# Performance work log

Measured on AMD Instinct MI355X. Metric: run time of the kernel, lower is better.

The kernel has to match this reference:

```python
import jax, jax.numpy as jnp
import numpy as np

DIM = 1024
HEADS = 32
HEAD_DIM = DIM // HEADS
SR_RATIO = 2
N_RATIO = SR_RATIO * SR_RATIO  # AvgPool1d kernel/stride
BN_EPS = 1e-6


def setup_inputs() -> dict:
    key = jax.random.key(0)
    ks = jax.random.split(key, 10)
    B, N, C = 4, 2048, DIM
    s = C ** -0.5
    return {
        "x": jax.random.normal(ks[0], (B, N, C), dtype=jnp.float32),
        # torch.nn.Linear weights, shape [out, in]; applied as x @ W.T
        "Wq": jax.random.normal(ks[1], (C, C), dtype=jnp.float32) * s,
        "Wk": jax.random.normal(ks[2], (C, C), dtype=jnp.float32) * s,
        "Wv": jax.random.normal(ks[3], (C, C), dtype=jnp.float32) * s,
        "Wp": jax.random.normal(ks[4], (C, C), dtype=jnp.float32) * s,
        "bp": jax.random.normal(ks[5], (C,), dtype=jnp.float32) * 0.01,
        # BatchNorm1d (eval mode) affine + running stats over channel dim C
        "bn_gamma": jnp.ones((C,), dtype=jnp.float32),
        "bn_beta": jnp.zeros((C,), dtype=jnp.float32),
        "bn_mean": jax.random.normal(ks[6], (C,), dtype=jnp.float32) * 0.01,
        "bn_var": jnp.ones((C,), dtype=jnp.float32) + jax.random.uniform(ks[7], (C,), dtype=jnp.float32) * 0.1,
    }


def reference(x, Wq, Wk, Wv, Wp, bp, bn_gamma, bn_beta, bn_mean, bn_var):
    B, N, C = x.shape
    scale = HEAD_DIM ** -0.5
    # Q from full-resolution tokens
    q = (x @ Wq.T).reshape(B, N, HEADS, HEAD_DIM).transpose(0, 2, 1, 3)  # [B,H,N,d]
    # spatial reduction: AvgPool1d(kernel=N_RATIO, stride=N_RATIO) over tokens
    xr = x.reshape(B, N // N_RATIO, N_RATIO, C).mean(axis=2)  # [B,M,C]
    # BatchNorm1d eval: normalize channel dim with running stats
    xr = (xr - bn_mean) * jax.lax.rsqrt(bn_var + BN_EPS) * bn_gamma + bn_beta
    M = xr.shape[1]
    k = (xr @ Wk.T).reshape(B, M, HEADS, HEAD_DIM).transpose(0, 2, 1, 3)  # [B,H,M,d]
    v = (xr @ Wv.T).reshape(B, M, HEADS, HEAD_DIM).transpose(0, 2, 1, 3)  # [B,H,M,d]
    # NOTE: no softmax in the original module — raw scaled scores feed the second matmul
    attn = jnp.einsum("bhnd,bhmd->bhnm", q, k) * scale  # [B,H,N,M]
    out = jnp.einsum("bhnm,bhmd->bhnd", attn, v)        # [B,H,N,d]
    out = out.transpose(0, 2, 1, 3).reshape(B, N, C)
    return out @ Wp.T + bp
```

## Files before the change

### kernel.cpp

```cpp
#include <hip/hip_runtime.h>
#include <stdint.h>

#define DEVFN __device__ __forceinline__

typedef __attribute__((ext_vector_type(8))) short s16x8;
typedef __attribute__((ext_vector_type(4))) float f32x4;

DEVFN float bf2f(uint16_t u) {
  union { uint32_t i; float f; } v; v.i = ((uint32_t)u) << 16; return v.f;
}
DEVFN uint16_t f2bf(float f) {
  union { float f; uint32_t i; } v; v.f = f;
  uint32_t u = v.i;
  return (uint16_t)((u + 0x7FFFu + ((u >> 16) & 1u)) >> 16);
}

DEVFN void gload_lds16(const void* g, void* l) {
  __builtin_amdgcn_global_load_lds(
      (const __attribute__((address_space(1))) uint32_t*)g,
      (__attribute__((address_space(3))) uint32_t*)l, 16, 0, 0);
}

__global__ __launch_bounds__(256)
void prep_kernel(const float* __restrict__ x,
                 const float* __restrict__ bn_g, const float* __restrict__ bn_b,
                 const float* __restrict__ bn_m, const float* __restrict__ bn_v,
                 const float* __restrict__ Wk, const float* __restrict__ Wv,
                 const float* __restrict__ Wp,
                 uint16_t* __restrict__ Xh,
                 uint16_t* __restrict__ XRh,
                 uint16_t* __restrict__ Wkvi,
                 uint16_t* __restrict__ Wph)
{
  const int t = threadIdx.x;
  const int bid = blockIdx.x;
  if (bid < 2048) {
    const int prow = bid;
    const int c0 = t * 4;
    const size_t xbase = (size_t)prow * 4096 + c0;
    float s[4] = {0.f, 0.f, 0.f, 0.f};
#pragma unroll
    for (int r = 0; r < 4; ++r) {
      const float4 w = *(const float4*)(x + xbase + (size_t)r * 1024);
      const float vv[4] = { w.x, w.y, w.z, w.w };
      uint64_t wh = 0;
#pragma unroll
      for (int j = 0; j < 4; ++j) {
        wh |= ((uint64_t)f2bf(vv[j])) << (16 * j);
        s[j] += vv[j];
      }
      *(uint64_t*)(Xh + xbase + (size_t)r * 1024) = wh;
    }
    uint64_t wh = 0;
#pragma unroll
    for (int j = 0; j < 4; ++j) {
      const int c = c0 + j;
      const float y = (s[j] * 0.25f - bn_m[c]) / sqrtf(bn_v[c] + 1e-6f) * bn_g[c] + bn_b[c];
      wh |= ((uint64_t)f2bf(y)) << (16 * j);
    }
    *(uint64_t*)(XRh + (size_t)prow * 1024 + c0) = wh;
  } else {
    const int wb = bid - 2048;
    const int which = wb >> 10;
    const int i = (wb & 1023) * 256 + t;
    const float* src = (which == 0) ? Wk : (which == 1) ? Wv : Wp;
    const float4 v = ((const float4*)src)[i];
    const float vv[4] = { v.x, v.y, v.z, v.w };
    uint64_t wh = 0;
#pragma unroll
    for (int j = 0; j < 4; ++j)
      wh |= ((uint64_t)f2bf(vv[j])) << (16 * j);
    if (which == 2) {
      ((uint64_t*)Wph)[i] = wh;
    } else {
      const int row  = i >> 8;
      const int col4 = i & 255;
      const int nrow = ((row >> 5) << 6) + which * 32 + (row & 31);
      ((uint64_t*)Wkvi)[(size_t)nrow * 256 + col4] = wh;
    }
  }
}

template<int APARTS, int BPARTS, bool BATCHB, bool AMODA, int EPI, bool KSPLIT2,
         bool SMALLM>
__global__ __launch_bounds__(256, 2)
void gemm_nt(const uint16_t* __restrict__ A0, const uint16_t* __restrict__ A1,
             const uint16_t* __restrict__ B0, const uint16_t* __restrict__ B1,
             float* __restrict__ C32, uint16_t* __restrict__ Cb0,
             const float* __restrict__ bias,
             int M, int N, int K, int rows_per_batch)
{
  constexpr int BM = SMALLM ? 64 : 128, BN = 128, BK = 64;
  constexpr int WCN = SMALLM ? 4 : 2;
  constexpr int WNW = BN / WCN;
  constexpr int NREP = WNW / 16;
  constexpr int APASS = SMALLM ? 2 : 4;
  __shared__ uint16_t sA[APARTS][BM * BK];
  __shared__ uint16_t sB[BPARTS][BN * BK];

  const int t = threadIdx.x;
  const int lane = t & 63;
  const int wave = t >> 6;
  const int wr = wave / WCN, wc = wave % WCN;
  const int fq = lane >> 4, fr = lane & 15;

  const int nwg = gridDim.x;
  const int cpx = nwg >> 3;
  const int orig = blockIdx.x;
  const int swz = (orig & 7) * cpx + (orig >> 3);
  const int nbx = N >> 7;
  const int bm = (swz / nbx) * BM;
  const int bn = (swz % nbx) * BN;

  const uint16_t* Ap[2] = { A0, A1 };
  const uint16_t* Bp[2] = { B0, B1 };
  if (BATCHB) {
    const size_t boff = (size_t)(bm / rows_per_batch) * (size_t)N * (size_t)K;
    Bp[0] += boff;
    if (BPARTS > 1) Bp[1] += boff;
  }
  if (KSPLIT2) {
    const size_t half = (size_t)blockIdx.y * M * N;
    if (EPI == 1) Cb0 += half; else C32 += half;
  }

  f32x4 acc[4][NREP];
#pragma unroll
  for (int m = 0; m < 4; ++m)
#pragma unroll
    for (int n = 0; n < NREP; ++n) acc[m][n] = (f32x4)0.0f;

  const int nkt = K >> (KSPLIT2 ? 7 : 6);
  const int kt0 = KSPLIT2 ? (blockIdx.y * nkt) : 0;
  for (int kt = kt0; kt < kt0 + nkt; ++kt) {
    __syncthreads();
#pragma unroll
    for (int i = 0; i < APASS; ++i) {
      const int X = t * 16 + i * 4096;
      const int r = X >> 7;
      const int g = ((X >> 4) & 7) ^ (r & 7);
      const int kcol = (kt << 6) + g * 8;
      const int arow = AMODA ? ((bm + r) & 1023) : (bm + r);
      const size_t srcA = (size_t)arow * K + kcol;
#pragma unroll
      for (int p = 0; p < APARTS; ++p)
        gload_lds16(Ap[p] + srcA, (char*)(&sA[p][0]) + X);
    }
#pragma unroll
    for (int i = 0; i < 4; ++i) {
      const int X = t * 16 + i * 4096;
      const int r = X >> 7;
      const int g = ((X >> 4) & 7) ^ (r & 7);
      const int kcol = (kt << 6) + g * 8;
      const size_t srcB = (size_t)(bn + r) * K + kcol;
#pragma unroll
      for (int p = 0; p < BPARTS; ++p)
        gload_lds16(Bp[p] + srcB, (char*)(&sB[p][0]) + X);
    }
    __syncthreads();
#pragma unroll
    for (int ks = 0; ks < 2; ++ks) {
      s16x8 av[APARTS][4], bv[BPARTS][NREP];
#pragma unroll
      for (int m = 0; m < 4; ++m) {
        const int ra = wr * 64 + m * 16 + fr;
        const int offA = ra * 128 + ((((ks << 2) + fq) ^ (ra & 7)) << 4);
#pragma unroll
        for (int p = 0; p < APARTS; ++p)
          av[p][m] = *(const s16x8*)((const char*)(&sA[p][0]) + offA);
      }
#pragma unroll
      for (int n = 0; n < NREP; ++n) {
        const int rb = wc * WNW + n * 16 + fr;
        const int offB = rb * 128 + ((((ks << 2) + fq) ^ (rb & 7)) << 4);
#pragma unroll
        for (int p = 0; p < BPARTS; ++p)
          bv[p][n] = *(const s16x8*)((const char*)(&sB[p][0]) + offB);
      }
#pragma unroll
      for (int m = 0; m < 4; ++m)
#pragma unroll
        for (int n = 0; n < NREP; ++n) {
          acc[m][n] = __builtin_amdgcn_mfma_f32_16x16x32_bf16(
              av[0][m], bv[0][n], acc[m][n], 0, 0, 0);
          if constexpr (BPARTS > 1)
            acc[m][n] = __builtin_amdgcn_mfma_f32_16x16x32_bf16(
                av[0][m], bv[1][n], acc[m][n], 0, 0, 0);
          if constexpr (APARTS > 1)
            acc[m][n] = __builtin_amdgcn_mfma_f32_16x16x32_bf16(
                av[1][m], bv[0][n], acc[m][n], 0, 0, 0);
        }
    }
  }

#pragma unroll
  for (int m = 0; m < 4; ++m) {
#pragma unroll
    for (int n = 0; n < NREP; ++n) {
#pragma unroll
      for (int j = 0; j < 4; ++j) {
        const int row = bm + wr * 64 + m * 16 + fq * 4 + j;
        const int col = bn + wc * WNW + n * 16 + fr;
        const size_t idx = (size_t)row * N + col;
        float v = acc[m][n][j];
        if constexpr (EPI == 0) {
          C32[idx] = v;
        } else if constexpr (EPI == 1) {
          Cb0[idx] = f2bf(v);
        } else {
          C32[idx] = v + bias[col];
        }
      }
    }
  }
}

__global__ __launch_bounds__(256, 2)
void gemm_kv(const uint16_t* __restrict__ A,
             const uint16_t* __restrict__ B,
             float* __restrict__ part)
{
  constexpr int BM = 64, BN = 128, BK = 64;
  __shared__ union {
    struct { uint16_t a[BM * BK]; uint16_t b[BN * BK]; } s;
    float c[BM][BN];
  } sm;

  const int t = threadIdx.x;
  const int lane = t & 63;
  const int wave = t >> 6;
  const int wc = wave;
  const int fq = lane >> 4, fr = lane & 15;

  const int nwg = gridDim.x;
  const int cpx = nwg >> 3;
  const int orig = blockIdx.x;
  const int swz = (orig & 7) * cpx + (orig >> 3);
  const int bmI = swz >> 4;
  const int bnI = swz & 15;
  const int bm = bmI * BM;
  const int bn = bnI * BN;

  f32x4 acc[4][2];
#pragma unroll
  for (int m = 0; m < 4; ++m)
#pragma unroll
    for (int n = 0; n < 2; ++n) acc[m][n] = (f32x4)0.0f;

  for (int kt = 0; kt < 16; ++kt) {
    __syncthreads();
#pragma unroll
    for (int i = 0; i < 2; ++i) {
      const int X = t * 16 + i * 4096;
      const int r = X >> 7;
      const int g = ((X >> 4) & 7) ^ (r & 7);
      const int kcol = (kt << 6) + g * 8;
      gload_lds16(A + (size_t)(bm + r) * 1024 + kcol, (char*)(&sm.s.a[0]) + X);
    }
#pragma unroll
    for (int i = 0; i < 4; ++i) {
      const int X = t * 16 + i * 4096;
      const int r = X >> 7;
      const int g = ((X >> 4) & 7) ^ (r & 7);
      const int kcol = (kt << 6) + g * 8;
      gload_lds16(B + (size_t)(bn + r) * 1024 + kcol, (char*)(&sm.s.b[0]) + X);
    }
    __syncthreads();
#pragma unroll
    for (int ks = 0; ks < 2; ++ks) {
      s16x8 av[4], bv[2];
#pragma unroll
      for (int m = 0; m < 4; ++m) {
        const int ra = m * 16 + fr;
        const int offA = ra * 128 + ((((ks << 2) + fq) ^ (ra & 7)) << 4);
        av[m] = *(const s16x8*)((const char*)(&sm.s.a[0]) + offA);
      }
#pragma unroll
      for (int n = 0; n < 2; ++n) {
        const int rb = wc * 32 + n * 16 + fr;
        const int offB = rb * 128 + ((((ks << 2) + fq) ^ (rb & 7)) << 4);
        bv[n] = *(const s16x8*)((const char*)(&sm.s.b[0]) + offB);
      }
#pragma unroll
      for (int m = 0; m < 4; ++m)
#pragma unroll
        for (int n = 0; n < 2; ++n)
          acc[m][n] = __builtin_amdgcn_mfma_f32_16x16x32_bf16(
              av[m], bv[n], acc[m][n], 0, 0, 0);
    }
  }

  __syncthreads();
#pragma unroll
  for (int m = 0; m < 4; ++m)
#pragma unroll
    for (int n = 0; n < 2; ++n)
#pragma unroll
      for (int j = 0; j < 4; ++j) {
        const int row = m * 16 + fq * 4 + j;
        const int col = wc * 32 + n * 16 + fr;
        sm.c[row][col] = acc[m][n][j];
      }
  __syncthreads();

  const int hsel = t >> 7;
  const int f  = (t >> 2) & 31;
  const int e0 = (t & 3) * 8;
  const int kcol = hsel * 64 + f;
  const int vcol = hsel * 64 + 32 + e0;
  f32x4 a0 = (f32x4)0.0f, a1 = (f32x4)0.0f;
#pragma unroll 8
  for (int m = 0; m < 64; ++m) {
    const float kf = sm.c[m][kcol];
    const f32x4 v0 = *(const f32x4*)&sm.c[m][vcol];
    const f32x4 v1 = *(const f32x4*)&sm.c[m][vcol + 4];
    a0 += v0 * kf;
    a1 += v1 * kf;
  }
  const int b = bmI >> 3, ch = bmI & 7;
  const int h = bnI * 2 + hsel;
  float* o = part + (((size_t)(b * 32 + h) * 8 + ch) * 32 + f) * 32 + e0;
  *(f32x4*)o = a0;
  *(f32x4*)(o + 4) = a1;
}

__global__ __launch_bounds__(256)
void t_kernel(const float* __restrict__ part, const float* __restrict__ Wq,
              uint16_t* __restrict__ Tth)
{
  const int bid = blockIdx.x;
  const int b = bid >> 7, h = (bid >> 2) & 31, cc = bid & 3;
  const int bh = b * 32 + h;
  const int t = threadIdx.x;
  __shared__ float sKV[32][32];
  {
    const int f = t >> 3, e0 = (t & 7) * 4;
    f32x4 a = (f32x4)0.0f;
#pragma unroll
    for (int ch = 0; ch < 8; ++ch)
      a += *(const f32x4*)(part + ((size_t)(bh * 8 + ch) * 32 + f) * 32 + e0);
    a *= 0.17677669529663687f;
    *(f32x4*)&sKV[f][e0] = a;
  }
  __syncthreads();
  const int c = cc * 256 + t;
  f32x4 acc[8];
#pragma unroll
  for (int i = 0; i < 8; ++i) acc[i] = (f32x4)0.0f;
  const float* wqp = Wq + (size_t)(h * 32) * 1024 + c;
#pragma unroll 8
  for (int f = 0; f < 32; ++f) {
    const float wq = wqp[(size_t)f * 1024];
#pragma unroll
    for (int i = 0; i < 8; ++i) {
      const f32x4 kv = *(const f32x4*)&sKV[f][i * 4];
      acc[i] += kv * wq;
    }
  }
  const size_t o = (((size_t)b << 10) + c) * 1024 + h * 32;
#pragma unroll
  for (int i = 0; i < 8; ++i) {
    uint64_t wh = 0;
#pragma unroll
    for (int j = 0; j < 4; ++j)
      wh |= ((uint64_t)f2bf(acc[i][j])) << (16 * j);
    *(uint64_t*)(Tth + o + i * 4) = wh;
  }
}

extern "C" void kernel_launch(void* const* d_in, const int* in_sizes, int n_in,
                              void* d_out, int out_size, void* d_ws, size_t ws_size,
                              hipStream_t stream)
{
  const float* x   = (const float*)d_in[0];
  const float* Wq  = (const float*)d_in[1];
  const float* Wk  = (const float*)d_in[2];
  const float* Wv  = (const float*)d_in[3];
  const float* Wp  = (const float*)d_in[4];
  const float* bp  = (const float*)d_in[5];
  const float* bng = (const float*)d_in[6];
  const float* bnb = (const float*)d_in[7];
  const float* bnm = (const float*)d_in[8];
  const float* bnv = (const float*)d_in[9];
  float* out = (float*)d_out;

  char* ws = (char*)d_ws;
  size_t off = 0;
  auto alloc = [&](size_t bytes) {
    char* p = ws + off;
    off += (bytes + 255) & ~(size_t)255;
    return p;
  };
  uint16_t* Xh   = (uint16_t*)alloc((size_t)8192 * 1024 * 2);
  uint16_t* XRh  = (uint16_t*)alloc((size_t)2048 * 1024 * 2);
  uint16_t* Wkvi = (uint16_t*)alloc((size_t)2048 * 1024 * 2);
  uint16_t* Wph  = (uint16_t*)alloc((size_t)1024 * 1024 * 2);
  uint16_t* Tth  = (uint16_t*)alloc((size_t)4096 * 1024 * 2);
  uint16_t* Gh   = (uint16_t*)alloc((size_t)4096 * 1024 * 2);
  float* KVpart = (float*)Gh;

  prep_kernel<<<5120, 256, 0, stream>>>(x, bng, bnb, bnm, bnv, Wk, Wv, Wp,
                                        Xh, XRh, Wkvi, Wph);
  gemm_kv<<<512, 256, 0, stream>>>(XRh, Wkvi, KVpart);
  t_kernel<<<512, 256, 0, stream>>>(KVpart, Wq, Tth);
  gemm_nt<1, 1, true, true, 1, false, true><<<512, 256, 0, stream>>>(
      Wph, nullptr, Tth, nullptr, nullptr, Gh, nullptr,
      4096, 1024, 1024, 1024);
  gemm_nt<1, 1, true, false, 2, false, false><<<512, 256, 0, stream>>>(
      Xh, nullptr, Gh, nullptr, out, nullptr, bp,
      8192, 1024, 1024, 2048);
}
```

Before: 99.90 us.

## Double K-tile depth to 128 in GEMMs and reshape KV tile to 128x64

Both GEMM kernels now stage a K-slice of 128 instead of 64 per iteration. This halves the number of barrier-separated load/compute rounds and doubles the MFMA work between syncs. The XOR swizzle is adjusted for the 256-byte LDS rows. gemm_kv is retiled from 64x128 to 128x64 with a 2x2 wave grid, so each block covers one head and two token chunks, and its KV reduction indexing is remapped. Unused multi-part and K-split template options are removed from gemm_nt. The larger LDS footprint (64KB for the big GEMM) may reduce occupancy below two blocks per CU.

```diff
diff --git a/kernel.cpp b/kernel.cpp
--- a/kernel.cpp
+++ b/kernel.cpp
@@ -81,22 +81,22 @@
   }
 }
 
-template<int APARTS, int BPARTS, bool BATCHB, bool AMODA, int EPI, bool KSPLIT2,
-         bool SMALLM>
+template<bool BATCHB, bool AMODA, int EPI, bool SMALLM>
 __global__ __launch_bounds__(256, 2)
-void gemm_nt(const uint16_t* __restrict__ A0, const uint16_t* __restrict__ A1,
-             const uint16_t* __restrict__ B0, const uint16_t* __restrict__ B1,
+void gemm_nt(const uint16_t* __restrict__ A0,
+             const uint16_t* __restrict__ B0,
              float* __restrict__ C32, uint16_t* __restrict__ Cb0,
              const float* __restrict__ bias,
              int M, int N, int K, int rows_per_batch)
 {
-  constexpr int BM = SMALLM ? 64 : 128, BN = 128, BK = 64;
+  constexpr int BM = SMALLM ? 64 : 128, BN = 128, BK = 128;
   constexpr int WCN = SMALLM ? 4 : 2;
   constexpr int WNW = BN / WCN;
   constexpr int NREP = WNW / 16;
-  constexpr int APASS = SMALLM ? 2 : 4;
-  __shared__ uint16_t sA[APARTS][BM * BK];
-  __shared__ uint16_t sB[BPARTS][BN * BK];
+  constexpr int APASS = SMALLM ? 4 : 8;
+  constexpr int BPASS = 8;
+  __shared__ uint16_t sA[BM * BK];
+  __shared__ uint16_t sB[BN * BK];
 
   const int t = threadIdx.x;
   const int lane = t & 63;
@@ -112,17 +112,10 @@
   const int bm = (swz / nbx) * BM;
   const int bn = (swz % nbx) * BN;
 
-  const uint16_t* Ap[2] = { A0, A1 };
-  const uint16_t* Bp[2] = { B0, B1 };
-  if (BATCHB) {
-    const size_t boff = (size_t)(bm / rows_per_batch) * (size_t)N * (size_t)K;
-    Bp[0] += boff;
-    if (BPARTS > 1) Bp[1] += boff;
-  }
-  if (KSPLIT2) {
-    const size_t half = (size_t)blockIdx.y * M * N;
-    if (EPI == 1) Cb0 += half; else C32 += half;
-  }
+  const uint16_t* Ap = A0;
+  const uint16_t* Bp = B0;
+  if (BATCHB)
+    Bp += (size_t)(bm / rows_per_batch) * (size_t)N * (size_t)K;
 
   f32x4 acc[4][NREP];
 #pragma unroll
@@ -130,66 +123,48 @@
 #pragma unroll
     for (int n = 0; n < NREP; ++n) acc[m][n] = (f32x4)0.0f;
 
-  const int nkt = K >> (KSPLIT2 ? 7 : 6);
-  const int kt0 = KSPLIT2 ? (blockIdx.y * nkt) : 0;
-  for (int kt = kt0; kt < kt0 + nkt; ++kt) {
+  const int nkt = K >> 7;
+  for (int kt = 0; kt < nkt; ++kt) {
     __syncthreads();
 #pragma unroll
     for (int i = 0; i < APASS; ++i) {
       const int X = t * 16 + i * 4096;
-      const int r = X >> 7;
-      const int g = ((X >> 4) & 7) ^ (r & 7);
-      const int kcol = (kt << 6) + g * 8;
+      const int r = X >> 8;
+      const int g = ((X >> 4) & 15) ^ (r & 7);
+      const int kcol = (kt << 7) + g * 8;
       const int arow = AMODA ? ((bm + r) & 1023) : (bm + r);
-      const size_t srcA = (size_t)arow * K + kcol;
-#pragma unroll
-      for (int p = 0; p < APARTS; ++p)
-        gload_lds16(Ap[p] + srcA, (char*)(&sA[p][0]) + X);
-    }
-#pragma unroll
-    for (int i = 0; i < 4; ++i) {
+      gload_lds16(Ap + (size_t)arow * K + kcol, (char*)(&sA[0]) + X);
+    }
+#pragma unroll
+    for (int i = 0; i < BPASS; ++i) {
       const int X = t * 16 + i * 4096;
-      const int r = X >> 7;
-      const int g = ((X >> 4) & 7) ^ (r & 7);
-      const int kcol = (kt << 6) + g * 8;
-      const size_t srcB = (size_t)(bn + r) * K + kcol;
-#pragma unroll
-      for (int p = 0; p < BPARTS; ++p)
-        gload_lds16(Bp[p] + srcB, (char*)(&sB[p][0]) + X);
+      const int r = X >> 8;
+      const int g = ((X >> 4) & 15) ^ (r & 7);
+      const int kcol = (kt << 7) + g * 8;
+      gload_lds16(Bp + (size_t)(bn + r) * K + kcol, (char*)(&sB[0]) + X);
     }
     __syncthreads();
 #pragma unroll
-    for (int ks = 0; ks < 2; ++ks) {
-      s16x8 av[APARTS][4], bv[BPARTS][NREP];
+    for (int ks = 0; ks < 4; ++ks) {
+      s16x8 av[4], bv[NREP];
 #pragma unroll
       for (int m = 0; m < 4; ++m) {
         const int ra = wr * 64 + m * 16 + fr;
-        const int offA = ra * 128 + ((((ks << 2) + fq) ^ (ra & 7)) << 4);
-#pragma unroll
-        for (int p = 0; p < APARTS; ++p)
-          av[p][m] = *(const s16x8*)((const char*)(&sA[p][0]) + offA);
+        const int offA = ra * 256 + ((((ks << 2) + fq) ^ (ra & 7)) << 4);
+        av[m] = *(const s16x8*)((const char*)(&sA[0]) + offA);
       }
 #pragma unroll
       for (int n = 0; n < NREP; ++n) {
         const int rb = wc * WNW + n * 16 + fr;
-        const int offB = rb * 128 + ((((ks << 2) + fq) ^ (rb & 7)) << 4);
-#pragma unroll
-        for (int p = 0; p < BPARTS; ++p)
-          bv[p][n] = *(const s16x8*)((const char*)(&sB[p][0]) + offB);
+        const int offB = rb * 256 + ((((ks << 2) + fq) ^ (rb & 7)) << 4);
+        bv[n] = *(const s16x8*)((const char*)(&sB[0]) + offB);
       }
 #pragma unroll
       for (int m = 0; m < 4; ++m)
 #pragma unroll
-        for (int n = 0; n < NREP; ++n) {
+        for (int n = 0; n < NREP; ++n)
           acc[m][n] = __builtin_amdgcn_mfma_f32_16x16x32_bf16(
-              av[0][m], bv[0][n], acc[m][n], 0, 0, 0);
-          if constexpr (BPARTS > 1)
-            acc[m][n] = __builtin_amdgcn_mfma_f32_16x16x32_bf16(
-                av[0][m], bv[1][n], acc[m][n], 0, 0, 0);
-          if constexpr (APARTS > 1)
-            acc[m][n] = __builtin_amdgcn_mfma_f32_16x16x32_bf16(
-                av[1][m], bv[0][n], acc[m][n], 0, 0, 0);
-        }
+              av[m], bv[n], acc[m][n], 0, 0, 0);
     }
   }
 
@@ -203,9 +178,7 @@
         const int col = bn + wc * WNW + n * 16 + fr;
         const size_t idx = (size_t)row * N + col;
         float v = acc[m][n][j];
-        if constexpr (EPI == 0) {
-          C32[idx] = v;
-        } else if constexpr (EPI == 1) {
+        if constexpr (EPI == 1) {
           Cb0[idx] = f2bf(v);
         } else {
           C32[idx] = v + bias[col];
@@ -220,7 +193,7 @@
              const uint16_t* __restrict__ B,
              float* __restrict__ part)
 {
-  constexpr int BM = 64, BN = 128, BK = 64;
+  constexpr int BM = 128, BN = 64, BK = 128;
   __shared__ union {
     struct { uint16_t a[BM * BK]; uint16_t b[BN * BK]; } s;
     float c[BM][BN];
@@ -229,15 +202,15 @@
   const int t = threadIdx.x;
   const int lane = t & 63;
   const int wave = t >> 6;
-  const int wc = wave;
+  const int wr = wave >> 1, wc = wave & 1;
   const int fq = lane >> 4, fr = lane & 15;
 
   const int nwg = gridDim.x;
   const int cpx = nwg >> 3;
   const int orig = blockIdx.x;
   const int swz = (orig & 7) * cpx + (orig >> 3);
-  const int bmI = swz >> 4;
-  const int bnI = swz & 15;
+  const int bmI = swz >> 5;
+  const int bnI = swz & 31;
   const int bm = bmI * BM;
   const int bn = bnI * BN;
 
@@ -247,38 +220,38 @@
 #pragma unroll
     for (int n = 0; n < 2; ++n) acc[m][n] = (f32x4)0.0f;
 
-  for (int kt = 0; kt < 16; ++kt) {
+  for (int kt = 0; kt < 8; ++kt) {
     __syncthreads();
 #pragma unroll
-    for (int i = 0; i < 2; ++i) {
+    for (int i = 0; i < 8; ++i) {
       const int X = t * 16 + i * 4096;
-      const int r = X >> 7;
-      const int g = ((X >> 4) & 7) ^ (r & 7);
-      const int kcol = (kt << 6) + g * 8;
+      const int r = X >> 8;
+      const int g = ((X >> 4) & 15) ^ (r & 7);
+      const int kcol = (kt << 7) + g * 8;
       gload_lds16(A + (size_t)(bm + r) * 1024 + kcol, (char*)(&sm.s.a[0]) + X);
     }
 #pragma unroll
     for (int i = 0; i < 4; ++i) {
       const int X = t * 16 + i * 4096;
-      const int r = X >> 7;
-      const int g = ((X >> 4) & 7) ^ (r & 7);
-      const int kcol = (kt << 6) + g * 8;
+      const int r = X >> 8;
+      const int g = ((X >> 4) & 15) ^ (r & 7);
+      const int kcol = (kt << 7) + g * 8;
       gload_lds16(B + (size_t)(bn + r) * 1024 + kcol, (char*)(&sm.s.b[0]) + X);
     }
     __syncthreads();
 #pragma unroll
-    for (int ks = 0; ks < 2; ++ks) {
+    for (int ks = 0; ks < 4; ++ks) {
       s16x8 av[4], bv[2];
 #pragma unroll
       for (int m = 0; m < 4; ++m) {
-        const int ra = m * 16 + fr;
-        const int offA = ra * 128 + ((((ks << 2) + fq) ^ (ra & 7)) << 4);
+        const int ra = wr * 64 + m * 16 + fr;
+        const int offA = ra * 256 + ((((ks << 2) + fq) ^ (ra & 7)) << 4);
         av[m] = *(const s16x8*)((const char*)(&sm.s.a[0]) + offA);
       }
 #pragma unroll
       for (int n = 0; n < 2; ++n) {
         const int rb = wc * 32 + n * 16 + fr;
-        const int offB = rb * 128 + ((((ks << 2) + fq) ^ (rb & 7)) << 4);
+        const int offB = rb * 256 + ((((ks << 2) + fq) ^ (rb & 7)) << 4);
         bv[n] = *(const s16x8*)((const char*)(&sm.s.b[0]) + offB);
       }
 #pragma unroll
@@ -297,28 +270,27 @@
     for (int n = 0; n < 2; ++n)
 #pragma unroll
       for (int j = 0; j < 4; ++j) {
-        const int row = m * 16 + fq * 4 + j;
+        const int row = wr * 64 + m * 16 + fq * 4 + j;
         const int col = wc * 32 + n * 16 + fr;
         sm.c[row][col] = acc[m][n][j];
       }
   __syncthreads();
 
-  const int hsel = t >> 7;
+  const int chs = t >> 7;
   const int f  = (t >> 2) & 31;
   const int e0 = (t & 3) * 8;
-  const int kcol = hsel * 64 + f;
-  const int vcol = hsel * 64 + 32 + e0;
   f32x4 a0 = (f32x4)0.0f, a1 = (f32x4)0.0f;
 #pragma unroll 8
-  for (int m = 0; m < 64; ++m) {
-    const float kf = sm.c[m][kcol];
-    const f32x4 v0 = *(const f32x4*)&sm.c[m][vcol];
-    const f32x4 v1 = *(const f32x4*)&sm.c[m][vcol + 4];
+  for (int mm = 0; mm < 64; ++mm) {
+    const int m = chs * 64 + mm;
+    const float kf = sm.c[m][f];
+    const f32x4 v0 = *(const f32x4*)&sm.c[m][32 + e0];
+    const f32x4 v1 = *(const f32x4*)&sm.c[m][36 + e0];
     a0 += v0 * kf;
     a1 += v1 * kf;
   }
-  const int b = bmI >> 3, ch = bmI & 7;
-  const int h = bnI * 2 + hsel;
+  const int b = bmI >> 2, ch = (bmI & 3) * 2 + chs;
+  const int h = bnI;
   float* o = part + (((size_t)(b * 32 + h) * 8 + ch) * 32 + f) * 32 + e0;
   *(f32x4*)o = a0;
   *(f32x4*)(o + 4) = a1;
@@ -403,10 +375,10 @@
                                         Xh, XRh, Wkvi, Wph);
   gemm_kv<<<512, 256, 0, stream>>>(XRh, Wkvi, KVpart);
   t_kernel<<<512, 256, 0, stream>>>(KVpart, Wq, Tth);
-  gemm_nt<1, 1, true, true, 1, false, true><<<512, 256, 0, stream>>>(
-      Wph, nullptr, Tth, nullptr, nullptr, Gh, nullptr,
+  gemm_nt<true, true, 1, true><<<512, 256, 0, stream>>>(
+      Wph, Tth, nullptr, Gh, nullptr,
       4096, 1024, 1024, 1024);
-  gemm_nt<1, 1, true, false, 2, false, false><<<512, 256, 0, stream>>>(
-      Xh, nullptr, Gh, nullptr, out, nullptr, bp,
+  gemm_nt<true, false, 2, false><<<512, 256, 0, stream>>>(
+      Xh, Gh, out, nullptr, bp,
       8192, 1024, 1024, 2048);
 }
```

After: 94.45 us. -5.5%, faster.
